# Performance work log

Hardware: AMD Instinct MI355X
Metric: run time of the kernel (lower is better)

Reference implementation:

```python
import jax, jax.numpy as jnp
import numpy as np

N, E, D, H, C, L = 10000, 160000, 512, 4, 128, 2  # nodes, edges, feat dim, heads, dim/head, layers


def setup_inputs() -> dict:
    key = jax.random.key(0)
    ks = jax.random.split(key, 16)
    s = 0.05  # weight scale (xavier-like)
    return {
        "x": jax.random.normal(ks[0], (N, D), jnp.float32),
        "edge_index": jax.random.randint(ks[1], (2, E), 0, N, dtype=jnp.int64),
        "edge_attr": jax.random.uniform(ks[2], (E, 1), jnp.float32),
        "Wq": jax.random.normal(ks[3], (L, D, H * C), jnp.float32) * s,
        "bq": jnp.zeros((L, H * C), jnp.float32),
        "Wk": jax.random.normal(ks[4], (L, D, H * C), jnp.float32) * s,
        "bk": jnp.zeros((L, H * C), jnp.float32),
        "Wv": jax.random.normal(ks[5], (L, D, H * C), jnp.float32) * s,
        "bv": jnp.zeros((L, H * C), jnp.float32),
        "We": jax.random.normal(ks[6], (L, 1, H * C), jnp.float32) * s,
        "Ws": jax.random.normal(ks[7], (L, D, H * C), jnp.float32) * s,
        "bs": jnp.zeros((L, H * C), jnp.float32),
        "gn_w": jnp.ones((L, H * C), jnp.float32),
        "gn_b": jnp.zeros((L, H * C), jnp.float32),
        "gn_ms": jnp.ones((L, H * C), jnp.float32),
    }


def _forward(x, edge_index, edge_attr, Wq, bq, Wk, bk, Wv, bv, We, Ws, bs, gn_w, gn_b, gn_ms):
    src, dst = edge_index[0], edge_index[1]
    h = x
    scale = 1.0 / jnp.sqrt(jnp.float32(C))
    for l in range(L):
        q = (h @ Wq[l] + bq[l]).reshape(N, H, C)
        k = (h @ Wk[l] + bk[l]).reshape(N, H, C)
        v = (h @ Wv[l] + bv[l]).reshape(N, H, C)
        e = (edge_attr @ We[l]).reshape(E, H, C)
        kj = k[src] + e                                    # [E,H,C]
        logits = jnp.einsum('ehc,ehc->eh', q[dst], kj) * scale  # [E,H]
        m = jax.ops.segment_max(logits, dst, num_segments=N)
        m = jnp.where(jnp.isfinite(m), m, 0.0)
        a = jnp.exp(logits - m[dst])
        denom = jax.ops.segment_sum(a, dst, num_segments=N)
        alpha = a / (denom[dst] + 1e-16)                   # scatter-softmax over in-edges
        msg = (v[src] + e) * alpha[:, :, None]             # [E,H,C]
        out = jax.ops.segment_sum(msg, dst, num_segments=N).reshape(N, H * C)
        out = out + h @ Ws[l] + bs[l]                      # root/skip connection
        # GraphNorm (single graph): mean over nodes
        mean = out.mean(0)
        sub = out - gn_ms[l] * mean
        var = (sub * sub).mean(0)
        out = gn_w[l] * sub * jax.lax.rsqrt(var + 1e-5) + gn_b[l]
        h = jax.nn.relu(out)
    xt = h.T @ h                                           # [D,D] gram matrix
    xt = (xt - xt.min()) / (xt.max() - xt.min() + 1e-8)
    iu = jnp.triu_indices(xt.shape[0], k=1)
    return xt[iu].reshape(-1, 1)


def reference(x, edge_index, edge_attr, Wq, bq, Wk, bk, Wv, bv, We, Ws, bs, gn_w, gn_b, gn_ms):
    return _forward(x, edge_index, edge_attr, Wq, bq, Wk, bk, Wv, bv, We, Ws, bs, gn_w, gn_b, gn_ms)
```

## Files before the change

kernel.cpp:

```cpp
#include <hip/hip_runtime.h>
#include <math.h>
#include <stdint.h>

typedef unsigned short u16;
typedef __attribute__((ext_vector_type(8))) _Float16 f16x8;
typedef __attribute__((ext_vector_type(4))) float f32x4;

constexpr int NN = 10000;
constexpr int NE = 160000;
constexpr int DD = 512;
constexpr int NL = 2;
constexpr int MPAD = 10112;
constexpr int K2 = 1024;
constexpr int NC = 2048;
constexpr int GZ = 32;
constexpr float SCALE = 0.08838834764831845f;

constexpr size_t B_C   = 0;
constexpr size_t B_XT  = (size_t)10016 * NC * 4;
constexpr size_t B_SM  = B_XT + (size_t)262144 * 4;
constexpr size_t B_A2  = B_SM + 32768;
constexpr size_t B_B2T = B_A2 + (size_t)MPAD * K2 * 2;
constexpr size_t B_INT = B_B2T + (size_t)2 * NC * K2 * 2;
constexpr size_t SM_CS = 0, SM_CQ = 512, SM_CA = 1024, SM_CB = 1536;
constexpr size_t SM_PMN = 2048, SM_PMX = 2304, SM_MM = 2560, SM_BIAS = 2688;
constexpr size_t I_INDPTR = 0;
constexpr size_t I_CNT    = 10016;
constexpr size_t I_CUR    = 20032;
constexpr size_t I_SSRC   = 30048;
constexpr size_t I_SATTR  = 190048;

__device__ __forceinline__ u16 f2h(float v) {
    _Float16 h = (_Float16)v;
    union { _Float16 h; u16 u; } x; x.h = h;
    return x.u;
}
__device__ __forceinline__ float h2f(u16 b) {
    union { u16 u; _Float16 h; } y; y.u = b;
    return (float)y.h;
}
__device__ __forceinline__ void gload16(const u16* g, u16* l) {
    __builtin_amdgcn_global_load_lds(
        (const __attribute__((address_space(1))) void*)g,
        (__attribute__((address_space(3))) void*)l, 16, 0, 0);
}
__device__ __forceinline__ void tile_pair(int p, int& ti, int& tj) {
    ti = (p < 4) ? 0 : (p < 7) ? 1 : (p < 9) ? 2 : 3;
    tj = p - ((ti == 0) ? 0 : (ti == 1) ? 3 : (ti == 2) ? 5 : 6);
}

__global__ void hist_kernel(const int* __restrict__ dst, int* __restrict__ cnt) {
    int e = blockIdx.x * 256 + threadIdx.x;
    if (e < NE) atomicAdd(&cnt[dst[e]], 1);
}

__global__ void scan_kernel(const int* __restrict__ cnt, int* __restrict__ indptr,
                            int* __restrict__ cur) {
    __shared__ int sh[1024];
    int tid = threadIdx.x;
    int carry = 0;
    for (int base = 0; base < NN; base += 1024) {
        int idx = base + tid;
        int v = (idx < NN) ? cnt[idx] : 0;
        sh[tid] = v;
        __syncthreads();
        #pragma unroll
        for (int off = 1; off < 1024; off <<= 1) {
            int t = (tid >= off) ? sh[tid - off] : 0;
            __syncthreads();
            sh[tid] += t;
            __syncthreads();
        }
        int incl = sh[tid];
        int excl = incl - v;
        if (idx < NN) { indptr[idx] = carry + excl; cur[idx] = carry + excl; }
        int total = sh[1023];
        __syncthreads();
        carry += total;
    }
    if (tid == 0) indptr[NN] = carry;
}

__global__ void scatter_kernel(const int* __restrict__ src, const int* __restrict__ dst,
                               const float* __restrict__ eattr, int* __restrict__ cur,
                               int* __restrict__ ssrc, float* __restrict__ sattr) {
    int e = blockIdx.x * 256 + threadIdx.x;
    if (e < NE) {
        int d = dst[e];
        int p = atomicAdd(&cur[d], 1);
        ssrc[p]  = src[e];
        sattr[p] = eattr[e];
    }
}

__global__ void convert_x_kernel(const float* __restrict__ x, u16* __restrict__ A2) {
    size_t idx = (size_t)blockIdx.x * 256 + threadIdx.x;
    if (idx >= (size_t)MPAD * 512) return;
    int r = (int)(idx >> 9), c = (int)(idx & 511);
    float v = (r < NN) ? x[(size_t)r * 512 + c] : 0.f;
    u16 hi = f2h(v);
    float lo = v - h2f(hi);
    u16* row = A2 + (size_t)r * K2;
    row[c] = hi; row[512 + c] = f2h(lo);
}

__global__ void convert_w_kernel(const float* __restrict__ Wq, const float* __restrict__ Wk,
                                 const float* __restrict__ Wv, const float* __restrict__ Ws,
                                 u16* __restrict__ B2T) {
    __shared__ float t[64][65];
    int bz = blockIdx.z; int l = bz >> 2, m = bz & 3;
    const float* W = (m == 0 ? Wq : m == 1 ? Wk : m == 2 ? Wv : Ws) + (size_t)l * 512 * 512;
    int k0 = blockIdx.x * 64, n0 = blockIdx.y * 64;
    int tx = threadIdx.x, ty = threadIdx.y;
    #pragma unroll
    for (int i = 0; i < 16; i++) {
        int kk = ty + 4 * i;
        t[kk][tx] = W[(size_t)(k0 + kk) * 512 + n0 + tx];
    }
    __syncthreads();
    u16* B = B2T + (size_t)l * NC * K2;
    #pragma unroll
    for (int i = 0; i < 16; i++) {
        int nn = ty + 4 * i;
        float v = t[tx][nn];
        u16 hi = f2h(v);
        u16* row = B + (size_t)(m * 512 + n0 + nn) * K2 + k0;
        row[tx] = hi; row[512 + tx] = hi;
    }
}

__global__ void convert_b_kernel(const float* __restrict__ bq, const float* __restrict__ bk,
                                 const float* __restrict__ bv, const float* __restrict__ bs,
                                 float* __restrict__ biascat) {
    int idx = blockIdx.x * 256 + threadIdx.x;
    if (idx >= 2 * NC) return;
    int l = idx >> 11, c = idx & 2047;
    int m = c >> 9, j = c & 511;
    const float* b = (m == 0 ? bq : m == 1 ? bk : m == 2 ? bv : bs);
    biascat[idx] = b[l * 512 + j];
}

__global__ __launch_bounds__(256) void gemm_mfma(
    const u16* __restrict__ A2, const u16* __restrict__ B2T,
    const float* __restrict__ biasc, float* __restrict__ C)
{
    __shared__ u16 As[4096];
    __shared__ u16 Bs[4096];
    int tid = threadIdx.x;
    int wave = tid >> 6, lane = tid & 63;
    int wr = wave >> 1, wc = wave & 1;

    int bid = blockIdx.x;
    int xcd = bid & 7, qq = bid >> 3;
    int half = (qq >= 79) ? 1 : 0;
    int mb = qq - half * 79;
    int nb = xcd * 2 + half;
    int row0 = mb * 128, col0 = nb * 128;
    int mtype = nb >> 2;

    int ar0 = tid >> 2;
    int ac0 = (tid & 3) * 8;
    const u16* gA = A2  + (size_t)(row0 + ar0) * K2 + ac0;
    const u16* gB = B2T + (size_t)(col0 + ar0) * K2 + ac0;
    u16* lA = &As[wave * 512];
    u16* lB = &Bs[wave * 512];

    f32x4 acc[4][4];
    #pragma unroll
    for (int m = 0; m < 4; ++m)
        #pragma unroll
        for (int n = 0; n < 4; ++n) acc[m][n] = (f32x4){0.f, 0.f, 0.f, 0.f};

    int frow = lane & 15, fk = (lane >> 4) * 8;

    for (int kt = 0; kt < K2 / 32; ++kt) {
        gload16(gA,             lA);
        gload16(gA + 64 * K2,   lA + 2048);
        gload16(gB,             lB);
        gload16(gB + 64 * K2,   lB + 2048);
        gA += 32; gB += 32;
        __syncthreads();
        f16x8 af[4], bfr[4];
        #pragma unroll
        for (int m = 0; m < 4; ++m)
            af[m] = *reinterpret_cast<const f16x8*>(&As[(wr * 64 + m * 16 + frow) * 32 + fk]);
        #pragma unroll
        for (int n = 0; n < 4; ++n)
            bfr[n] = *reinterpret_cast<const f16x8*>(&Bs[(wc * 64 + n * 16 + frow) * 32 + fk]);
        #pragma unroll
        for (int m = 0; m < 4; ++m)
            #pragma unroll
            for (int n = 0; n < 4; ++n)
                acc[m][n] = __builtin_amdgcn_mfma_f32_16x16x32_f16(af[m], bfr[n], acc[m][n], 0, 0, 0);
        __syncthreads();
    }

    u16* KV = (u16*)C;
    int rq = lane >> 4;
    #pragma unroll
    for (int n = 0; n < 4; ++n) {
        int gc = col0 + wc * 64 + n * 16 + frow;
        float bv = biasc[gc];
        #pragma unroll
        for (int m = 0; m < 4; ++m) {
            int gr0 = row0 + wr * 64 + m * 16 + rq * 4;
            #pragma unroll
            for (int r = 0; r < 4; ++r) {
                int gr = gr0 + r;
                if (gr < NN) {
                    float val = acc[m][n][r] + bv;
                    if (mtype == 0 || mtype == 3) C[(size_t)gr * NC + gc] = val;
                    else                          KV[(size_t)gr * 4096 + 512 + gc] = f2h(val);
                }
            }
        }
    }
}

__global__ __launch_bounds__(256) void agg_kernel(
    float* __restrict__ C, const float* __restrict__ Wel,
    const int* __restrict__ indptr, const int* __restrict__ ssrc,
    const float* __restrict__ sattr)
{
    int wid  = threadIdx.x >> 6;
    int lane = threadIdx.x & 63;
    int n = blockIdx.x * 4 + wid;
    if (n >= NN) return;
    int base = lane * 8;
    const u16* KV = (const u16*)C;

    const float4* qp = (const float4*)(C + (size_t)n * NC + base);
    float4 q0 = qp[0], q1 = qp[1];
    float qv[8] = {q0.x,q0.y,q0.z,q0.w,q1.x,q1.y,q1.z,q1.w};
    float we[8];
    #pragma unroll
    for (int j = 0; j < 8; j++) we[j] = Wel[base + j];

    float t = 0.f;
    #pragma unroll
    for (int j = 0; j < 8; j++) t = fmaf(qv[j], we[j], t);
    #pragma unroll
    for (int m = 1; m < 16; m <<= 1) t += __shfl_xor(t, m, 64);
    float qWe = t;

    float mrun = -1e30f, msum = 0.f, cattr = 0.f;
    float acc[8] = {0.f,0.f,0.f,0.f,0.f,0.f,0.f,0.f};
    int p0 = indptr[n], p1 = indptr[n + 1];
    for (int p = p0; p < p1; ++p) {
        int s = ssrc[p];
        float at = sattr[p];
        union { uint4 u; u16 h[8]; } kr, vr;
        kr.u = *(const uint4*)(KV + (size_t)s * 4096 + 1024 + base);
        float d = 0.f;
        #pragma unroll
        for (int j = 0; j < 8; j++) d = fmaf(qv[j], h2f(kr.h[j]), d);
        #pragma unroll
        for (int m = 1; m < 16; m <<= 1) d += __shfl_xor(d, m, 64);
        float logit = (d + at * qWe) * SCALE;
        float mnew = fmaxf(mrun, logit);
        float r = __expf(mrun - mnew);
        float a = __expf(logit - mnew);
        vr.u = *(const uint4*)(KV + (size_t)s * 4096 + 1536 + base);
        msum  = msum  * r + a;
        cattr = cattr * r + a * at;
        #pragma unroll
        for (int j = 0; j < 8; j++) acc[j] = acc[j] * r + a * h2f(vr.h[j]);
        mrun = mnew;
    }
    float inv = 1.f / (msum + 1e-16f);
    float* op = C + (size_t)n * NC + 1536 + base;
    float4 o0 = *(float4*)op, o1 = *(float4*)(op + 4);
    float ov[8] = {o0.x,o0.y,o0.z,o0.w,o1.x,o1.y,o1.z,o1.w};
    #pragma unroll
    for (int j = 0; j < 8; j++) ov[j] += (acc[j] + cattr * we[j]) * inv;
    *(float4*)op       = make_float4(ov[0], ov[1], ov[2], ov[3]);
    *(float4*)(op + 4) = make_float4(ov[4], ov[5], ov[6], ov[7]);
}

__global__ void colstat_kernel(const float* __restrict__ C,
                               float* __restrict__ cs, float* __restrict__ cq) {
    int c = threadIdx.x;
    int r0 = blockIdx.x * 125;
    float s0 = 0, s1 = 0, q0 = 0, q1 = 0;
    for (int r = r0; r < r0 + 125; ++r) {
        float v0 = C[(size_t)r * NC + 1536 + c];
        float v1 = C[(size_t)r * NC + 1536 + c + 256];
        s0 += v0; q0 += v0 * v0;
        s1 += v1; q1 += v1 * v1;
    }
    atomicAdd(&cs[c], s0);       atomicAdd(&cq[c], q0);
    atomicAdd(&cs[c + 256], s1); atomicAdd(&cq[c + 256], q1);
}

__global__ void coef_kernel(const float* __restrict__ cs, const float* __restrict__ cq,
                            const float* __restrict__ gnw, const float* __restrict__ gnb,
                            const float* __restrict__ gnm,
                            float* __restrict__ Aa, float* __restrict__ Bb) {
    int c = blockIdx.x * 256 + threadIdx.x;
    if (c >= DD) return;
    float mean = cs[c] * (1.f / NN);
    float ex2  = cq[c] * (1.f / NN);
    float ms = gnm[c];
    float var = ex2 - (2.f * ms - ms * ms) * mean * mean;
    float A = gnw[c] * rsqrtf(var + 1e-5f);
    Aa[c] = A;
    Bb[c] = gnb[c] - A * ms * mean;
}

__global__ void normrelu_kernel(const float* __restrict__ C, const float* __restrict__ Aa,
                                const float* __restrict__ Bb, u16* __restrict__ A2) {
    for (size_t idx = (size_t)blockIdx.x * 256 + threadIdx.x; idx < (size_t)NN * 512;
         idx += (size_t)2048 * 256) {
        int r = (int)(idx >> 9), c = (int)(idx & 511);
        float v = fmaxf(fmaf(Aa[c], C[(size_t)r * NC + 1536 + c], Bb[c]), 0.f);
        u16 hi = f2h(v);
        float lo = v - h2f(hi);
        u16* row = A2 + (size_t)r * K2;
        row[c] = hi; row[512 + c] = f2h(lo);
    }
}

__global__ __launch_bounds__(256) void gram_part_kernel(const u16* __restrict__ A2,
                                                        float* __restrict__ part) {
    __shared__ u16 LA[128][40], LB[128][40];
    int b = blockIdx.x;
    int p = b >> 5, z = b & (GZ - 1);
    int ti, tj; tile_pair(p, ti, tj);
    int i0c = ti * 128, j0c = tj * 128;
    int st0 = (z * 316) / GZ, st1 = ((z + 1) * 316) / GZ;

    int t = threadIdx.x;
    int c = t & 127, nb = t >> 7;
    int wave = t >> 6, lane = t & 63;
    int wr = wave >> 1, wc = wave & 1;
    int frow = lane & 15, fk = (lane >> 4) * 8, rq = lane >> 4;

    f32x4 acc[4][4];
    #pragma unroll
    for (int m = 0; m < 4; ++m)
        #pragma unroll
        for (int n = 0; n < 4; ++n) acc[m][n] = (f32x4){0.f, 0.f, 0.f, 0.f};

    for (int st = st0; st < st1; ++st) {
        int node0 = st * 32 + nb * 16;
        uint4 bufA4[2], bufB4[2];
        u16* ba = (u16*)bufA4; u16* bb = (u16*)bufB4;
        #pragma unroll
        for (int i = 0; i < 16; i++) {
            const u16* rp = A2 + (size_t)(node0 + i) * K2;
            ba[i] = rp[i0c + c];
            bb[i] = rp[j0c + c];
        }
        __syncthreads();
        *(uint4*)&LA[c][nb * 16]     = bufA4[0];
        *(uint4*)&LA[c][nb * 16 + 8] = bufA4[1];
        *(uint4*)&LB[c][nb * 16]     = bufB4[0];
        *(uint4*)&LB[c][nb * 16 + 8] = bufB4[1];
        __syncthreads();
        f16x8 af[4], bfr[4];
        #pragma unroll
        for (int m = 0; m < 4; ++m)
            af[m] = *reinterpret_cast<const f16x8*>(&LA[wr * 64 + m * 16 + frow][fk]);
        #pragma unroll
        for (int n = 0; n < 4; ++n)
            bfr[n] = *reinterpret_cast<const f16x8*>(&LB[wc * 64 + n * 16 + frow][fk]);
        #pragma unroll
        for (int m = 0; m < 4; ++m)
            #pragma unroll
            for (int n = 0; n < 4; ++n)
                acc[m][n] = __builtin_amdgcn_mfma_f32_16x16x32_f16(af[m], bfr[n], acc[m][n], 0, 0, 0);
    }

    float* pp = part + ((size_t)b << 14);
    #pragma unroll
    for (int m = 0; m < 4; ++m) {
        int li0 = wr * 64 + m * 16 + rq * 4;
        #pragma unroll
        for (int n = 0; n < 4; ++n) {
            int lj = wc * 64 + n * 16 + frow;
            #pragma unroll
            for (int r = 0; r < 4; ++r)
                pp[(li0 + r) * 128 + lj] = acc[m][n][r];
        }
    }
}

__global__ __launch_bounds__(256) void gram_reduce_kernel(const float* __restrict__ part,
                                                          float* __restrict__ xt,
                                                          float* __restrict__ pmn,
                                                          float* __restrict__ pmx) {
    __shared__ float smn[256], smx[256];
    int tid = threadIdx.x;
    int g = blockIdx.x * 1024 + tid * 4;
    int p = g >> 14, idx = g & 16383;
    const float* bp = part + ((size_t)p * GZ << 14) + idx;
    float4 s = make_float4(0.f, 0.f, 0.f, 0.f);
    #pragma unroll
    for (int z = 0; z < GZ; ++z) {
        float4 v = *(const float4*)(bp + (size_t)z * 16384);
        s.x += v.x; s.y += v.y; s.z += v.z; s.w += v.w;
    }
    int ti, tj; tile_pair(p, ti, tj);
    int li = idx >> 7, lj = idx & 127;
    *(float4*)&xt[(size_t)(ti * 128 + li) * DD + tj * 128 + lj] = s;
    float mn = fminf(fminf(s.x, s.y), fminf(s.z, s.w));
    float mx = fmaxf(fmaxf(s.x, s.y), fmaxf(s.z, s.w));
    smn[tid] = mn; smx[tid] = mx;
    __syncthreads();
    for (int st = 128; st > 0; st >>= 1) {
        if (tid < st) {
            smn[tid] = fminf(smn[tid], smn[tid + st]);
            smx[tid] = fmaxf(smx[tid], smx[tid + st]);
        }
        __syncthreads();
    }
    if (tid == 0) { pmn[blockIdx.x] = smn[0]; pmx[blockIdx.x] = smx[0]; }
}

__global__ void minmax2_kernel(const float* __restrict__ pmn, const float* __restrict__ pmx,
                               float* __restrict__ mm) {
    __shared__ float smn[256], smx[256];
    int tid = threadIdx.x;
    smn[tid] = (tid < 160) ? pmn[tid] : 1e30f;
    smx[tid] = (tid < 160) ? pmx[tid] : -1e30f;
    __syncthreads();
    for (int s = 128; s > 0; s >>= 1) {
        if (tid < s) { smn[tid] = fminf(smn[tid], smn[tid + s]); smx[tid] = fmaxf(smx[tid], smx[tid + s]); }
        __syncthreads();
    }
    if (tid == 0) { mm[0] = smn[0]; mm[1] = smx[0]; }
}

__global__ void final_kernel(const float* __restrict__ xt, const float* __restrict__ mm,
                             float* __restrict__ outp) {
    int idx = blockIdx.x * 256 + threadIdx.x;
    if (idx >= 262144) return;
    int i = idx >> 9, j = idx & 511;
    if (j <= i) return;
    float mn = mm[0], mx = mm[1];
    float v = (xt[idx] - mn) / (mx - mn + 1e-8f);
    int p = i * 511 - (i * (i - 1)) / 2 + (j - i - 1);
    outp[p] = v;
}

extern "C" void kernel_launch(void* const* d_in, const int* in_sizes, int n_in,
                              void* d_out, int out_size, void* d_ws, size_t ws_size,
                              hipStream_t stream) {
    const float* x     = (const float*)d_in[0];
    const int*   ei    = (const int*)d_in[1];
    const float* eattr = (const float*)d_in[2];
    const float* Wq = (const float*)d_in[3];  const float* bq = (const float*)d_in[4];
    const float* Wk = (const float*)d_in[5];  const float* bk = (const float*)d_in[6];
    const float* Wv = (const float*)d_in[7];  const float* bv = (const float*)d_in[8];
    const float* We = (const float*)d_in[9];
    const float* Ws = (const float*)d_in[10]; const float* bs = (const float*)d_in[11];
    const float* gnw = (const float*)d_in[12];
    const float* gnb = (const float*)d_in[13];
    const float* gnm = (const float*)d_in[14];

    char*  wsb = (char*)d_ws;
    float* C    = (float*)(wsb + B_C);
    float* xt   = (float*)(wsb + B_XT);
    float* sm   = (float*)(wsb + B_SM);
    u16*   A2   = (u16*)(wsb + B_A2);
    u16*   B2T  = (u16*)(wsb + B_B2T);
    int*   wsI  = (int*)(wsb + B_INT);

    const int* src = ei;
    const int* dst = ei + NE;

    convert_x_kernel<<<(MPAD * 512) / 256, 256, 0, stream>>>(x, A2);
    convert_w_kernel<<<dim3(8, 8, 8), dim3(64, 4), 0, stream>>>(Wq, Wk, Wv, Ws, B2T);
    convert_b_kernel<<<16, 256, 0, stream>>>(bq, bk, bv, bs, sm + SM_BIAS);

    hipMemsetAsync(wsI + I_CNT, 0, NN * sizeof(int), stream);
    hist_kernel<<<(NE + 255) / 256, 256, 0, stream>>>(dst, wsI + I_CNT);
    scan_kernel<<<1, 1024, 0, stream>>>(wsI + I_CNT, wsI + I_INDPTR, wsI + I_CUR);
    scatter_kernel<<<(NE + 255) / 256, 256, 0, stream>>>(src, dst, eattr, wsI + I_CUR,
                                                         wsI + I_SSRC, (float*)(wsI + I_SATTR));

    for (int l = 0; l < NL; ++l) {
        gemm_mfma<<<1264, 256, 0, stream>>>(A2, B2T + (size_t)l * NC * K2,
                                            sm + SM_BIAS + (size_t)l * NC, C);

        agg_kernel<<<2500, 256, 0, stream>>>(C, We + (size_t)l * DD,
                                             wsI + I_INDPTR, wsI + I_SSRC,
                                             (const float*)(wsI + I_SATTR));

        hipMemsetAsync(sm + SM_CS, 0, 1024 * sizeof(float), stream);
        colstat_kernel<<<80, 256, 0, stream>>>(C, sm + SM_CS, sm + SM_CQ);
        coef_kernel<<<2, 256, 0, stream>>>(sm + SM_CS, sm + SM_CQ,
                                           gnw + (size_t)l * DD, gnb + (size_t)l * DD,
                                           gnm + (size_t)l * DD, sm + SM_CA, sm + SM_CB);
        normrelu_kernel<<<2048, 256, 0, stream>>>(C, sm + SM_CA, sm + SM_CB, A2);
    }

    float* part = C;
    gram_part_kernel<<<10 * GZ, 256, 0, stream>>>(A2, part);
    gram_reduce_kernel<<<160, 256, 0, stream>>>(part, xt, sm + SM_PMN, sm + SM_PMX);
    minmax2_kernel<<<1, 256, 0, stream>>>(sm + SM_PMN, sm + SM_PMX, sm + SM_MM);
    final_kernel<<<1024, 256, 0, stream>>>(xt, sm + SM_MM, (float*)d_out);
}
```

Measured before the change: 405.6 us.

## Double-buffer LDS tiles in MFMA GEMM and XOR-swizzle to avoid bank conflicts

The GEMM main loop now uses two LDS buffers and prefetches the next K-tile with direct-to-LDS loads while MFMAs run on the current one. Waiting on vmcnt(4) with a raw s_barrier replaces the full __syncthreads. The K-chunk column index is also XOR-swizzled by row so that LDS fragment reads spread across banks. This doubles LDS use per block and relies on hand-written waitcnt counts being correct for the gload16 instruction count.

```diff
diff --git a/kernel.cpp b/kernel.cpp
--- a/kernel.cpp
+++ b/kernel.cpp
@@ -14,6 +14,7 @@
 constexpr int K2 = 1024;
 constexpr int NC = 2048;
 constexpr int GZ = 32;
+constexpr int NKT = K2 / 32;
 constexpr float SCALE = 0.08838834764831845f;
 
 constexpr size_t B_C   = 0;
@@ -144,8 +145,8 @@
     const u16* __restrict__ A2, const u16* __restrict__ B2T,
     const float* __restrict__ biasc, float* __restrict__ C)
 {
-    __shared__ u16 As[4096];
-    __shared__ u16 Bs[4096];
+    __shared__ u16 As[2][4096];
+    __shared__ u16 Bs[2][4096];
     int tid = threadIdx.x;
     int wave = tid >> 6, lane = tid & 63;
     int wr = wave >> 1, wc = wave & 1;
@@ -159,11 +160,18 @@
     int mtype = nb >> 2;
 
     int ar0 = tid >> 2;
-    int ac0 = (tid & 3) * 8;
+    int ac0 = (((tid & 3) ^ ((tid >> 2) & 3)) * 8);
     const u16* gA = A2  + (size_t)(row0 + ar0) * K2 + ac0;
     const u16* gB = B2T + (size_t)(col0 + ar0) * K2 + ac0;
-    u16* lA = &As[wave * 512];
-    u16* lB = &Bs[wave * 512];
+
+    auto stage = [&](int b, int kt) {
+        const u16* pa = gA + kt * 32;
+        const u16* pb = gB + kt * 32;
+        gload16(pa,            &As[b][wave * 512]);
+        gload16(pa + 64 * K2,  &As[b][wave * 512 + 2048]);
+        gload16(pb,            &Bs[b][wave * 512]);
+        gload16(pb + 64 * K2,  &Bs[b][wave * 512 + 2048]);
+    };
 
     f32x4 acc[4][4];
     #pragma unroll
@@ -172,27 +180,32 @@
         for (int n = 0; n < 4; ++n) acc[m][n] = (f32x4){0.f, 0.f, 0.f, 0.f};
 
     int frow = lane & 15, fk = (lane >> 4) * 8;
-
-    for (int kt = 0; kt < K2 / 32; ++kt) {
-        gload16(gA,             lA);
-        gload16(gA + 64 * K2,   lA + 2048);
-        gload16(gB,             lB);
-        gload16(gB + 64 * K2,   lB + 2048);
-        gA += 32; gB += 32;
-        __syncthreads();
+    int fks = fk ^ ((frow & 3) << 3);
+
+    stage(0, 0);
+    int buf = 0;
+    for (int kt = 0; kt < NKT; ++kt) {
+        if (kt < NKT - 1) {
+            stage(buf ^ 1, kt + 1);
+            asm volatile("s_waitcnt vmcnt(4)" ::: "memory");
+        } else {
+            asm volatile("s_waitcnt vmcnt(0)" ::: "memory");
+        }
+        __builtin_amdgcn_s_barrier();
         f16x8 af[4], bfr[4];
         #pragma unroll
         for (int m = 0; m < 4; ++m)
-            af[m] = *reinterpret_cast<const f16x8*>(&As[(wr * 64 + m * 16 + frow) * 32 + fk]);
+            af[m] = *reinterpret_cast<const f16x8*>(&As[buf][(wr * 64 + m * 16 + frow) * 32 + fks]);
         #pragma unroll
         for (int n = 0; n < 4; ++n)
-            bfr[n] = *reinterpret_cast<const f16x8*>(&Bs[(wc * 64 + n * 16 + frow) * 32 + fk]);
+            bfr[n] = *reinterpret_cast<const f16x8*>(&Bs[buf][(wc * 64 + n * 16 + frow) * 32 + fks]);
         #pragma unroll
         for (int m = 0; m < 4; ++m)
             #pragma unroll
             for (int n = 0; n < 4; ++n)
                 acc[m][n] = __builtin_amdgcn_mfma_f32_16x16x32_f16(af[m], bfr[n], acc[m][n], 0, 0, 0);
-        __syncthreads();
+        __builtin_amdgcn_s_barrier();
+        buf ^= 1;
     }
 
     u16* KV = (u16*)C;
```

Result: slower. 424.7 us (+4.7%).

## Stage fp16 Q/K/V epilogue through LDS for coalesced stores; store Q as fp16

Applied to the files above, without the earlier changes.

The GEMM epilogue for Q, K and V tiles now writes fp16 results into shared memory and then issues 16-byte coalesced row stores. Previously each lane scattered individual 2-byte stores. Q is now kept in fp16 in the packed KV buffer instead of fp32, and the K/V offsets shift to match. The aggregation kernel therefore reads Q as a single 16-byte load. This reduces scattered global writes and Q read bandwidth, at the cost of extra LDS barriers in the epilogue and fp16 precision on Q.

```diff
diff --git a/kernel.cpp b/kernel.cpp
--- a/kernel.cpp
+++ b/kernel.cpp
@@ -14,6 +14,7 @@
 constexpr int K2 = 1024;
 constexpr int NC = 2048;
 constexpr int GZ = 32;
+constexpr int NKT = K2 / 32;
 constexpr float SCALE = 0.08838834764831845f;
 
 constexpr size_t B_C   = 0;
@@ -173,7 +174,7 @@
 
     int frow = lane & 15, fk = (lane >> 4) * 8;
 
-    for (int kt = 0; kt < K2 / 32; ++kt) {
+    for (int kt = 0; kt < NKT; ++kt) {
         gload16(gA,             lA);
         gload16(gA + 64 * K2,   lA + 2048);
         gload16(gB,             lB);
@@ -195,24 +196,55 @@
         __syncthreads();
     }
 
-    u16* KV = (u16*)C;
     int rq = lane >> 4;
-    #pragma unroll
-    for (int n = 0; n < 4; ++n) {
-        int gc = col0 + wc * 64 + n * 16 + frow;
-        float bv = biasc[gc];
-        #pragma unroll
-        for (int m = 0; m < 4; ++m) {
-            int gr0 = row0 + wr * 64 + m * 16 + rq * 4;
+    if (mtype == 3) {
+        #pragma unroll
+        for (int n = 0; n < 4; ++n) {
+            int gc = col0 + wc * 64 + n * 16 + frow;
+            float bv = biasc[gc];
             #pragma unroll
-            for (int r = 0; r < 4; ++r) {
-                int gr = gr0 + r;
-                if (gr < NN) {
-                    float val = acc[m][n][r] + bv;
-                    if (mtype == 0 || mtype == 3) C[(size_t)gr * NC + gc] = val;
-                    else                          KV[(size_t)gr * 4096 + 512 + gc] = f2h(val);
+            for (int m = 0; m < 4; ++m) {
+                int gr0 = row0 + wr * 64 + m * 16 + rq * 4;
+                #pragma unroll
+                for (int r = 0; r < 4; ++r) {
+                    int gr = gr0 + r;
+                    if (gr < NN) C[(size_t)gr * NC + gc] = acc[m][n][r] + bv;
                 }
             }
+        }
+    } else {
+        u16* KV = (u16*)C;
+        size_t colbase = (size_t)mtype * 512 + (size_t)(nb & 3) * 128;
+        float bvv[4];
+        #pragma unroll
+        for (int n = 0; n < 4; ++n) bvv[n] = biasc[col0 + wc * 64 + n * 16 + frow];
+        #pragma unroll
+        for (int p = 0; p < 4; ++p) {
+            if (wr == (p >> 1)) {
+                int mb0 = (p & 1) * 2;
+                #pragma unroll
+                for (int mm = 0; mm < 2; ++mm) {
+                    int lr0 = mm * 16 + rq * 4;
+                    #pragma unroll
+                    for (int n = 0; n < 4; ++n) {
+                        int col = wc * 64 + n * 16 + frow;
+                        #pragma unroll
+                        for (int r = 0; r < 4; ++r)
+                            As[(lr0 + r) * 128 + col] = f2h(acc[mb0 + mm][n][r] + bvv[n]);
+                    }
+                }
+            }
+            __syncthreads();
+            #pragma unroll
+            for (int i = 0; i < 2; ++i) {
+                int cid = tid + 256 * i;
+                int lr = cid >> 4, seg = cid & 15;
+                int gr = row0 + p * 32 + lr;
+                if (gr < NN)
+                    *(uint4*)(KV + (size_t)gr * 4096 + colbase + seg * 8) =
+                        *(const uint4*)&As[lr * 128 + seg * 8];
+            }
+            __syncthreads();
         }
     }
 }
@@ -229,9 +261,11 @@
     int base = lane * 8;
     const u16* KV = (const u16*)C;
 
-    const float4* qp = (const float4*)(C + (size_t)n * NC + base);
-    float4 q0 = qp[0], q1 = qp[1];
-    float qv[8] = {q0.x,q0.y,q0.z,q0.w,q1.x,q1.y,q1.z,q1.w};
+    union { uint4 u; u16 h[8]; } qr;
+    qr.u = *(const uint4*)(KV + (size_t)n * 4096 + base);
+    float qv[8];
+    #pragma unroll
+    for (int j = 0; j < 8; j++) qv[j] = h2f(qr.h[j]);
     float we[8];
     #pragma unroll
     for (int j = 0; j < 8; j++) we[j] = Wel[base + j];
@@ -250,7 +284,7 @@
         int s = ssrc[p];
         float at = sattr[p];
         union { uint4 u; u16 h[8]; } kr, vr;
-        kr.u = *(const uint4*)(KV + (size_t)s * 4096 + 1024 + base);
+        kr.u = *(const uint4*)(KV + (size_t)s * 4096 + 512 + base);
         float d = 0.f;
         #pragma unroll
         for (int j = 0; j < 8; j++) d = fmaf(qv[j], h2f(kr.h[j]), d);
@@ -260,7 +294,7 @@
         float mnew = fmaxf(mrun, logit);
         float r = __expf(mrun - mnew);
         float a = __expf(logit - mnew);
-        vr.u = *(const uint4*)(KV + (size_t)s * 4096 + 1536 + base);
+        vr.u = *(const uint4*)(KV + (size_t)s * 4096 + 1024 + base);
         msum  = msum  * r + a;
         cattr = cattr * r + a * at;
         #pragma unroll
```

Result: slower. 447.7 us (+10.4%).
